# Kernel optimization log

Measured on AMD Instinct MI355X. Metric: run time of the kernel, lower is better.

The kernel has to match this reference:

```python
import jax, jax.numpy as jnp
import numpy as np

EPS = 1e-5

def _ln(x, g, b):
    mu = jnp.mean(x, axis=-1, keepdims=True)
    var = jnp.mean((x - mu) ** 2, axis=-1, keepdims=True)
    return (x - mu) / jnp.sqrt(var + EPS) * g + b

def setup_inputs() -> dict:
    key = jax.random.key(0)
    ks = jax.random.split(key, 8)
    S, B, L, M, D, Nq, H = 4, 256, 256, 4, 512, 4, 2048
    G = (M + 2) * D
    inp = {
        'ns_tokens': jax.random.normal(ks[0], (B, M, D), jnp.float32),
        'seq_tokens': jax.random.normal(ks[1], (S, B, L, D), jnp.float32),
        'seq_padding_masks': jax.random.randint(ks[2], (S, B, L), 0, 2).astype(bool),
        'seq_stats': jax.random.normal(ks[3], (S, B, 6), jnp.float32),
        'gin_gamma': jnp.ones((G,), jnp.float32),
        'gin_beta': jnp.zeros((G,), jnp.float32),
        'stat_W': 0.02 * jax.random.normal(ks[4], (S, 6, D), jnp.float32),
        'stat_b': jnp.zeros((S, D), jnp.float32),
        'stat_ln_g': jnp.ones((S, D), jnp.float32),
        'stat_ln_b': jnp.zeros((S, D), jnp.float32),
        'W1': 0.02 * jax.random.normal(ks[5], (S, Nq, G, H), jnp.float32),
        'b1': jnp.zeros((S, Nq, H), jnp.float32),
        'W2': 0.02 * jax.random.normal(ks[6], (S, Nq, H, D), jnp.float32),
        'b2': jnp.zeros((S, Nq, D), jnp.float32),
        'ln_g': jnp.ones((S, Nq, D), jnp.float32),
        'ln_b': jnp.zeros((S, Nq, D), jnp.float32),
    }
    return inp

def reference(ns_tokens, seq_tokens, seq_padding_masks, seq_stats,
              gin_gamma, gin_beta, stat_W, stat_b, stat_ln_g, stat_ln_b,
              W1, b1, W2, b2, ln_g, ln_b):
    S, B = seq_tokens.shape[0], ns_tokens.shape[0]
    ns_flat = ns_tokens.reshape(B, -1)                       # (B, M*D)
    valid = (~seq_padding_masks).astype(seq_tokens.dtype)[..., None]  # (S,B,L,1)
    denom = jnp.clip(jnp.sum(valid, axis=2), 1.0)            # (S,B,1)
    pooled = jnp.sum(seq_tokens * valid, axis=2) / denom     # (S,B,D)
    stat = jnp.einsum('sbf,sfd->sbd', seq_stats, stat_W) + stat_b[:, None]
    stat = _ln(stat, stat_ln_g[:, None], stat_ln_b[:, None])  # (S,B,D)
    gi = jnp.concatenate([jnp.broadcast_to(ns_flat[None], (S, B, ns_flat.shape[1])), pooled, stat], axis=-1)
    gi = _ln(gi, gin_gamma, gin_beta)                        # (S,B,G)
    h = jax.nn.silu(jnp.einsum('sbg,sqgh->sqbh', gi, W1) + b1[:, :, None])
    q = jnp.einsum('sqbh,sqhd->sqbd', h, W2) + b2[:, :, None]
    q = _ln(q, ln_g[:, :, None], ln_b[:, :, None])           # (S,Nq,B,D)
    return jnp.transpose(q, (0, 2, 1, 3))                    # (S,B,Nq,D)
```

## Files before the change

### kernel.cpp

```cpp
#include <hip/hip_runtime.h>
#include <hip/hip_bf16.h>

#define S_ 4
#define B_ 256
#define L_ 256
#define D_ 512
#define NQ_ 4
#define H_ 2048
#define G_ 3072

typedef __attribute__((ext_vector_type(4))) float f32x4;
typedef __attribute__((ext_vector_type(8))) short s16x8;

__device__ __forceinline__ unsigned short f2bf(float x) {
    __hip_bfloat16 hb = __float2bfloat16(x);
    return reinterpret_cast<unsigned short&>(hb);
}

__device__ __forceinline__ float block_sum256(float v, float* red) {
    #pragma unroll
    for (int off = 32; off > 0; off >>= 1) v += __shfl_down(v, off, 64);
    int tid = threadIdx.x;
    int lane = tid & 63, wid = tid >> 6;
    if (lane == 0) red[wid] = v;
    __syncthreads();
    float r = (tid < 4) ? red[tid] : 0.f;
    #pragma unroll
    for (int off = 4; off > 0; off >>= 1) r += __shfl_down(r, off, 64);
    if (tid == 0) red[0] = r;
    __syncthreads();
    float out = red[0];
    __syncthreads();
    return out;
}

__global__ __launch_bounds__(256) void pool_kernel(
    const float* __restrict__ seq_tokens,
    const unsigned char* __restrict__ masks_raw,
    float* __restrict__ pooled)
{
    const int sb = blockIdx.x;
    const int tid = threadIdx.x;
    __shared__ float sval[L_];
    __shared__ float scount[4];
    __shared__ f32x4 spart[256];
    __shared__ int is_bool_flag;

    if (tid == 0) is_bool_flag = 0;
    __syncthreads();
    {
        unsigned int w = reinterpret_cast<const unsigned int*>(masks_raw)[tid];
        if (w & 0xFFFFFF00u) is_bool_flag = 1;
    }
    __syncthreads();
    const bool is_bool = (is_bool_flag != 0);

    int mval;
    if (is_bool) {
        mval = masks_raw[(size_t)sb * L_ + tid];
    } else {
        mval = reinterpret_cast<const int*>(masks_raw)[(size_t)sb * L_ + tid];
    }
    float valid = mval ? 0.f : 1.f;
    sval[tid] = valid;
    float c = valid;
    #pragma unroll
    for (int off = 32; off > 0; off >>= 1) c += __shfl_down(c, off, 64);
    if ((tid & 63) == 0) scount[tid >> 6] = c;
    __syncthreads();
    const float denom = fmaxf(scount[0] + scount[1] + scount[2] + scount[3], 1.f);

    const float* base = seq_tokens + (size_t)sb * L_ * D_;
    const int cidx = tid & 127;
    const int rg = tid >> 7;
    f32x4 acc = {0.f, 0.f, 0.f, 0.f};
    for (int l = rg; l < L_; l += 2) {
        float vl = sval[l];
        f32x4 v = *reinterpret_cast<const f32x4*>(base + (size_t)l * D_ + cidx * 4);
        acc += v * vl;
    }
    spart[tid] = acc;
    __syncthreads();
    if (tid < 128) {
        f32x4 r = spart[tid] + spart[tid + 128];
        r *= (1.f / denom);
        *reinterpret_cast<f32x4*>(pooled + (size_t)sb * D_ + cidx * 4) = r;
    }
}

__global__ __launch_bounds__(256) void gi_kernel(
    const float* __restrict__ ns_tokens,
    const float* __restrict__ seq_stats,
    const float* __restrict__ stat_W,
    const float* __restrict__ stat_b,
    const float* __restrict__ stat_ln_g,
    const float* __restrict__ stat_ln_b,
    const float* __restrict__ gin_gamma,
    const float* __restrict__ gin_beta,
    const float* __restrict__ pooled,
    __hip_bfloat16* __restrict__ gi)
{
    const int sb = blockIdx.x;
    const int s = sb >> 8;
    const int b = sb & 255;
    const int tid = threadIdx.x;
    __shared__ float red[8];
    __shared__ float sstat[D_];

    float st[6];
    #pragma unroll
    for (int f = 0; f < 6; ++f) st[f] = seq_stats[(size_t)sb * 6 + f];

    float sp[2];
    #pragma unroll
    for (int k = 0; k < 2; ++k) {
        int d = tid + k * 256;
        float a = stat_b[s * D_ + d];
        #pragma unroll
        for (int f = 0; f < 6; ++f) a += st[f] * stat_W[(s * 6 + f) * D_ + d];
        sp[k] = a;
    }
    float ssum = block_sum256(sp[0] + sp[1], red);
    float ssq  = block_sum256(sp[0] * sp[0] + sp[1] * sp[1], red);
    float mu = ssum / D_;
    float var = ssq / D_ - mu * mu;
    float rinv = rsqrtf(var + 1e-5f);
    #pragma unroll
    for (int k = 0; k < 2; ++k) {
        int d = tid + k * 256;
        sstat[d] = (sp[k] - mu) * rinv * stat_ln_g[s * D_ + d] + stat_ln_b[s * D_ + d];
    }
    __syncthreads();

    float gv[12];
    float gsum = 0.f, gsq = 0.f;
    #pragma unroll
    for (int k = 0; k < 12; ++k) {
        int g = tid + k * 256;
        float v;
        if (g < 2048)       v = ns_tokens[(size_t)b * 2048 + g];
        else if (g < 2560)  v = pooled[(size_t)sb * D_ + (g - 2048)];
        else                v = sstat[g - 2560];
        gv[k] = v;
        gsum += v;
        gsq += v * v;
    }
    gsum = block_sum256(gsum, red);
    gsq  = block_sum256(gsq, red);
    mu = gsum / G_;
    var = gsq / G_ - mu * mu;
    rinv = rsqrtf(var + 1e-5f);
    #pragma unroll
    for (int k = 0; k < 12; ++k) {
        int g = tid + k * 256;
        float o = (gv[k] - mu) * rinv * gin_gamma[g] + gin_beta[g];
        gi[(size_t)sb * G_ + g] = __float2bfloat16(o);
    }
}

__global__ __launch_bounds__(256) void gemm1_kernel(
    const __hip_bfloat16* __restrict__ gi,
    const float* __restrict__ W1,
    const float* __restrict__ b1,
    __hip_bfloat16* __restrict__ hbuf)
{
    const int ntile = blockIdx.x;
    const int sq = blockIdx.y;
    const int s = sq >> 2;
    const int tid = threadIdx.x;
    const int lane = tid & 63;
    const int wid = tid >> 6;

    __shared__ __align__(16) unsigned short As[256 * 64];
    __shared__ __align__(16) unsigned short Ws[64 * 64];

    const __hip_bfloat16* Ab = gi + (size_t)s * B_ * G_;
    const float* Wb = W1 + (size_t)sq * G_ * H_ + ntile * 64;

    f32x4 acc[4][4];
    #pragma unroll
    for (int i = 0; i < 4; ++i)
        #pragma unroll
        for (int j = 0; j < 4; ++j) acc[i][j] = (f32x4){0.f, 0.f, 0.f, 0.f};

    const int wn0 = (tid & 15) * 4;
    const int wk0 = (tid >> 4) * 4;

    for (int kt = 0; kt < G_ / 64; ++kt) {
        const int kbase = kt * 64;
        __syncthreads();
        #pragma unroll
        for (int i = 0; i < 8; ++i) {
            int slot = i * 256 + tid;
            int row = slot >> 3, cc = slot & 7;
            int swz = (row ^ (row >> 3)) & 7;
            s16x8 v = *reinterpret_cast<const s16x8*>(Ab + (size_t)row * G_ + kbase + cc * 8);
            *reinterpret_cast<s16x8*>(&As[row * 64 + ((cc ^ swz) * 8)]) = v;
        }
        float wv[4][4];
        #pragma unroll
        for (int kk = 0; kk < 4; ++kk) {
            f32x4 t = *reinterpret_cast<const f32x4*>(Wb + (size_t)(kbase + wk0 + kk) * H_ + wn0);
            #pragma unroll
            for (int j = 0; j < 4; ++j) wv[kk][j] = t[j];
        }
        #pragma unroll
        for (int nn = 0; nn < 4; ++nn) {
            int row = wn0 + nn;
            int swz = (row ^ (row >> 3)) & 7;
            unsigned long long pk =
                (unsigned long long)f2bf(wv[0][nn]) |
                ((unsigned long long)f2bf(wv[1][nn]) << 16) |
                ((unsigned long long)f2bf(wv[2][nn]) << 32) |
                ((unsigned long long)f2bf(wv[3][nn]) << 48);
            int byteoff = (row * 128 + wk0 * 2) ^ (swz << 4);
            *reinterpret_cast<unsigned long long*>(reinterpret_cast<char*>(Ws) + byteoff) = pk;
        }
        __syncthreads();
        #pragma unroll
        for (int kb = 0; kb < 2; ++kb) {
            s16x8 af[4], bfr[4];
            #pragma unroll
            for (int mi = 0; mi < 4; ++mi) {
                int r = wid * 64 + mi * 16 + (lane & 15);
                int swz = (r ^ (r >> 3)) & 7;
                int chunk = ((lane >> 4) + kb * 4) ^ swz;
                af[mi] = *reinterpret_cast<const s16x8*>(&As[r * 64 + chunk * 8]);
            }
            #pragma unroll
            for (int ni = 0; ni < 4; ++ni) {
                int r = ni * 16 + (lane & 15);
                int swz = (r ^ (r >> 3)) & 7;
                int chunk = ((lane >> 4) + kb * 4) ^ swz;
                bfr[ni] = *reinterpret_cast<const s16x8*>(&Ws[r * 64 + chunk * 8]);
            }
            #pragma unroll
            for (int mi = 0; mi < 4; ++mi)
                #pragma unroll
                for (int ni = 0; ni < 4; ++ni)
                    acc[mi][ni] = __builtin_amdgcn_mfma_f32_16x16x32_bf16(af[mi], bfr[ni], acc[mi][ni], 0, 0, 0);
        }
    }
    const float* b1p = b1 + (size_t)sq * H_ + ntile * 64;
    __hip_bfloat16* hp = hbuf + (size_t)sq * B_ * H_;
    #pragma unroll
    for (int mi = 0; mi < 4; ++mi)
        #pragma unroll
        for (int ni = 0; ni < 4; ++ni)
            #pragma unroll
            for (int r = 0; r < 4; ++r) {
                int row = wid * 64 + mi * 16 + ((lane >> 4) << 2) + r;
                int coll = ni * 16 + (lane & 15);
                float x = acc[mi][ni][r] + b1p[coll];
                float sg = 1.f / (1.f + __expf(-x));
                hp[(size_t)row * H_ + ntile * 64 + coll] = __float2bfloat16(x * sg);
            }
}

__global__ __launch_bounds__(256) void gemm2_kernel(
    const __hip_bfloat16* __restrict__ hbuf,
    const float* __restrict__ W2,
    float* __restrict__ qpre)
{
    const int ntile = blockIdx.x;
    const int mtile = blockIdx.y;
    const int sq = blockIdx.z;
    const int tid = threadIdx.x;
    const int lane = tid & 63;
    const int wid = tid >> 6;
    const int wm = wid >> 1, wn = wid & 1;

    __shared__ __align__(16) unsigned short As[128 * 64];
    __shared__ __align__(16) unsigned short Ws[64 * 64];

    const __hip_bfloat16* Ab = hbuf + ((size_t)sq * B_ + mtile * 128) * H_;
    const float* Wb = W2 + (size_t)sq * H_ * D_ + ntile * 64;

    f32x4 acc[4][2];
    #pragma unroll
    for (int i = 0; i < 4; ++i)
        #pragma unroll
        for (int j = 0; j < 2; ++j) acc[i][j] = (f32x4){0.f, 0.f, 0.f, 0.f};

    const int wn0 = (tid & 15) * 4;
    const int wk0 = (tid >> 4) * 4;

    for (int kt = 0; kt < H_ / 64; ++kt) {
        const int kbase = kt * 64;
        __syncthreads();
        #pragma unroll
        for (int i = 0; i < 4; ++i) {
            int slot = i * 256 + tid;
            int row = slot >> 3, cc = slot & 7;
            int swz = (row ^ (row >> 3)) & 7;
            s16x8 v = *reinterpret_cast<const s16x8*>(Ab + (size_t)row * H_ + kbase + cc * 8);
            *reinterpret_cast<s16x8*>(&As[row * 64 + ((cc ^ swz) * 8)]) = v;
        }
        float wv[4][4];
        #pragma unroll
        for (int kk = 0; kk < 4; ++kk) {
            f32x4 t = *reinterpret_cast<const f32x4*>(Wb + (size_t)(kbase + wk0 + kk) * D_ + wn0);
            #pragma unroll
            for (int j = 0; j < 4; ++j) wv[kk][j] = t[j];
        }
        #pragma unroll
        for (int nn = 0; nn < 4; ++nn) {
            int row = wn0 + nn;
            int swz = (row ^ (row >> 3)) & 7;
            unsigned long long pk =
                (unsigned long long)f2bf(wv[0][nn]) |
                ((unsigned long long)f2bf(wv[1][nn]) << 16) |
                ((unsigned long long)f2bf(wv[2][nn]) << 32) |
                ((unsigned long long)f2bf(wv[3][nn]) << 48);
            int byteoff = (row * 128 + wk0 * 2) ^ (swz << 4);
            *reinterpret_cast<unsigned long long*>(reinterpret_cast<char*>(Ws) + byteoff) = pk;
        }
        __syncthreads();
        #pragma unroll
        for (int kb = 0; kb < 2; ++kb) {
            s16x8 af[4], bfr[2];
            #pragma unroll
            for (int mi = 0; mi < 4; ++mi) {
                int r = wm * 64 + mi * 16 + (lane & 15);
                int swz = (r ^ (r >> 3)) & 7;
                int chunk = ((lane >> 4) + kb * 4) ^ swz;
                af[mi] = *reinterpret_cast<const s16x8*>(&As[r * 64 + chunk * 8]);
            }
            #pragma unroll
            for (int ni = 0; ni < 2; ++ni) {
                int r = wn * 32 + ni * 16 + (lane & 15);
                int swz = (r ^ (r >> 3)) & 7;
                int chunk = ((lane >> 4) + kb * 4) ^ swz;
                bfr[ni] = *reinterpret_cast<const s16x8*>(&Ws[r * 64 + chunk * 8]);
            }
            #pragma unroll
            for (int mi = 0; mi < 4; ++mi)
                #pragma unroll
                for (int ni = 0; ni < 2; ++ni)
                    acc[mi][ni] = __builtin_amdgcn_mfma_f32_16x16x32_bf16(af[mi], bfr[ni], acc[mi][ni], 0, 0, 0);
        }
    }
    #pragma unroll
    for (int mi = 0; mi < 4; ++mi)
        #pragma unroll
        for (int ni = 0; ni < 2; ++ni)
            #pragma unroll
            for (int r = 0; r < 4; ++r) {
                int row = mtile * 128 + wm * 64 + mi * 16 + ((lane >> 4) << 2) + r;
                int col = ntile * 64 + wn * 32 + ni * 16 + (lane & 15);
                qpre[((size_t)sq * B_ + row) * D_ + col] = acc[mi][ni][r];
            }
}

__global__ __launch_bounds__(256) void lnout_kernel(
    const float* __restrict__ qpre,
    const float* __restrict__ b2,
    const float* __restrict__ lng,
    const float* __restrict__ lnb,
    float* __restrict__ out)
{
    const int idx = blockIdx.x;
    const int sq = idx >> 8;
    const int b = idx & 255;
    const int tid = threadIdx.x;
    __shared__ float red[8];

    float v[2];
    #pragma unroll
    for (int k = 0; k < 2; ++k) {
        int d = tid + k * 256;
        v[k] = qpre[(size_t)idx * D_ + d] + b2[sq * D_ + d];
    }
    float sum = block_sum256(v[0] + v[1], red);
    float sq2 = block_sum256(v[0] * v[0] + v[1] * v[1], red);
    float mu = sum / D_;
    float var = sq2 / D_ - mu * mu;
    float rinv = rsqrtf(var + 1e-5f);
    const int s = sq >> 2, q = sq & 3;
    #pragma unroll
    for (int k = 0; k < 2; ++k) {
        int d = tid + k * 256;
        float o = (v[k] - mu) * rinv * lng[sq * D_ + d] + lnb[sq * D_ + d];
        out[(((size_t)s * B_ + b) * NQ_ + q) * D_ + d] = o;
    }
}

extern "C" void kernel_launch(void* const* d_in, const int* in_sizes, int n_in,
                              void* d_out, int out_size, void* d_ws, size_t ws_size,
                              hipStream_t stream) {
    const float* ns_tokens   = (const float*)d_in[0];
    const float* seq_tokens  = (const float*)d_in[1];
    const unsigned char* masks = (const unsigned char*)d_in[2];
    const float* seq_stats   = (const float*)d_in[3];
    const float* gin_gamma   = (const float*)d_in[4];
    const float* gin_beta    = (const float*)d_in[5];
    const float* stat_W      = (const float*)d_in[6];
    const float* stat_b      = (const float*)d_in[7];
    const float* stat_ln_g   = (const float*)d_in[8];
    const float* stat_ln_b   = (const float*)d_in[9];
    const float* W1          = (const float*)d_in[10];
    const float* b1          = (const float*)d_in[11];
    const float* W2          = (const float*)d_in[12];
    const float* b2          = (const float*)d_in[13];
    const float* ln_g        = (const float*)d_in[14];
    const float* ln_b        = (const float*)d_in[15];
    float* out = (float*)d_out;

    char* ws = (char*)d_ws;
    float* pooled        = (float*)(ws);
    __hip_bfloat16* gi   = (__hip_bfloat16*)(ws + 2097152);
    __hip_bfloat16* hbuf = (__hip_bfloat16*)(ws + 2097152 + 6291456);
    float* qpre          = (float*)(ws + 2097152 + 6291456 + 16777216);

    pool_kernel<<<dim3(S_ * B_), dim3(256), 0, stream>>>(seq_tokens, masks, pooled);
    gi_kernel<<<dim3(S_ * B_), dim3(256), 0, stream>>>(ns_tokens, seq_stats, stat_W, stat_b,
                                                       stat_ln_g, stat_ln_b, gin_gamma, gin_beta,
                                                       pooled, gi);
    gemm1_kernel<<<dim3(H_ / 64, S_ * NQ_), dim3(256), 0, stream>>>(gi, W1, b1, hbuf);
    gemm2_kernel<<<dim3(D_ / 64, B_ / 128, S_ * NQ_), dim3(256), 0, stream>>>(hbuf, W2, qpre);
    lnout_kernel<<<dim3(S_ * NQ_ * B_), dim3(256), 0, stream>>>(qpre, b2, ln_g, ln_b, out);
}
```

Measured before the change: 268.3 us.

## Remap GEMM blocks per XCD, issue weight loads first, store qpre as bf16

Both GEMM kernels switch to a 1D grid and remap block ids so that consecutive ids handled by the same XCD (bid & 7) share the same sq slice. This aims to improve L2 reuse of the shared activation tile across the XCDs. Inside the K loop, the fp32 weight global loads are now issued before the bf16 activation loads to expose more memory-level parallelism. The intermediate qpre buffer is stored as bf16 instead of fp32, halving its write and read traffic but adding rounding error before the final layernorm.

```diff
diff --git a/kernel.cpp b/kernel.cpp
--- a/kernel.cpp
+++ b/kernel.cpp
@@ -56,11 +56,8 @@
     const bool is_bool = (is_bool_flag != 0);
 
     int mval;
-    if (is_bool) {
-        mval = masks_raw[(size_t)sb * L_ + tid];
-    } else {
-        mval = reinterpret_cast<const int*>(masks_raw)[(size_t)sb * L_ + tid];
-    }
+    if (is_bool) mval = masks_raw[(size_t)sb * L_ + tid];
+    else         mval = reinterpret_cast<const int*>(masks_raw)[(size_t)sb * L_ + tid];
     float valid = mval ? 0.f : 1.f;
     sval[tid] = valid;
     float c = valid;
@@ -164,8 +161,10 @@
     const float* __restrict__ b1,
     __hip_bfloat16* __restrict__ hbuf)
 {
-    const int ntile = blockIdx.x;
-    const int sq = blockIdx.y;
+    const int bid = blockIdx.x;
+    const int wg = (bid & 7) * 64 + (bid >> 3);
+    const int ntile = wg & 31;
+    const int sq = wg >> 5;
     const int s = sq >> 2;
     const int tid = threadIdx.x;
     const int lane = tid & 63;
@@ -189,6 +188,13 @@
     for (int kt = 0; kt < G_ / 64; ++kt) {
         const int kbase = kt * 64;
         __syncthreads();
+        float wv[4][4];
+        #pragma unroll
+        for (int kk = 0; kk < 4; ++kk) {
+            f32x4 t = *reinterpret_cast<const f32x4*>(Wb + (size_t)(kbase + wk0 + kk) * H_ + wn0);
+            #pragma unroll
+            for (int j = 0; j < 4; ++j) wv[kk][j] = t[j];
+        }
         #pragma unroll
         for (int i = 0; i < 8; ++i) {
             int slot = i * 256 + tid;
@@ -196,13 +202,6 @@
             int swz = (row ^ (row >> 3)) & 7;
             s16x8 v = *reinterpret_cast<const s16x8*>(Ab + (size_t)row * G_ + kbase + cc * 8);
             *reinterpret_cast<s16x8*>(&As[row * 64 + ((cc ^ swz) * 8)]) = v;
-        }
-        float wv[4][4];
-        #pragma unroll
-        for (int kk = 0; kk < 4; ++kk) {
-            f32x4 t = *reinterpret_cast<const f32x4*>(Wb + (size_t)(kbase + wk0 + kk) * H_ + wn0);
-            #pragma unroll
-            for (int j = 0; j < 4; ++j) wv[kk][j] = t[j];
         }
         #pragma unroll
         for (int nn = 0; nn < 4; ++nn) {
@@ -260,11 +259,13 @@
 __global__ __launch_bounds__(256) void gemm2_kernel(
     const __hip_bfloat16* __restrict__ hbuf,
     const float* __restrict__ W2,
-    float* __restrict__ qpre)
+    __hip_bfloat16* __restrict__ qpre)
 {
-    const int ntile = blockIdx.x;
-    const int mtile = blockIdx.y;
-    const int sq = blockIdx.z;
+    const int bid = blockIdx.x;
+    const int wg = (bid & 7) * 32 + (bid >> 3);
+    const int ntile = wg & 7;
+    const int mtile = (wg >> 3) & 1;
+    const int sq = wg >> 4;
     const int tid = threadIdx.x;
     const int lane = tid & 63;
     const int wid = tid >> 6;
@@ -288,6 +289,13 @@
     for (int kt = 0; kt < H_ / 64; ++kt) {
         const int kbase = kt * 64;
         __syncthreads();
+        float wv[4][4];
+        #pragma unroll
+        for (int kk = 0; kk < 4; ++kk) {
+            f32x4 t = *reinterpret_cast<const f32x4*>(Wb + (size_t)(kbase + wk0 + kk) * D_ + wn0);
+            #pragma unroll
+            for (int j = 0; j < 4; ++j) wv[kk][j] = t[j];
+        }
         #pragma unroll
         for (int i = 0; i < 4; ++i) {
             int slot = i * 256 + tid;
@@ -295,13 +303,6 @@
             int swz = (row ^ (row >> 3)) & 7;
             s16x8 v = *reinterpret_cast<const s16x8*>(Ab + (size_t)row * H_ + kbase + cc * 8);
             *reinterpret_cast<s16x8*>(&As[row * 64 + ((cc ^ swz) * 8)]) = v;
-        }
-        float wv[4][4];
-        #pragma unroll
-        for (int kk = 0; kk < 4; ++kk) {
-            f32x4 t = *reinterpret_cast<const f32x4*>(Wb + (size_t)(kbase + wk0 + kk) * D_ + wn0);
-            #pragma unroll
-            for (int j = 0; j < 4; ++j) wv[kk][j] = t[j];
         }
         #pragma unroll
         for (int nn = 0; nn < 4; ++nn) {
@@ -348,12 +349,12 @@
             for (int r = 0; r < 4; ++r) {
                 int row = mtile * 128 + wm * 64 + mi * 16 + ((lane >> 4) << 2) + r;
                 int col = ntile * 64 + wn * 32 + ni * 16 + (lane & 15);
-                qpre[((size_t)sq * B_ + row) * D_ + col] = acc[mi][ni][r];
+                qpre[((size_t)sq * B_ + row) * D_ + col] = __float2bfloat16(acc[mi][ni][r]);
             }
 }
 
 __global__ __launch_bounds__(256) void lnout_kernel(
-    const float* __restrict__ qpre,
+    const __hip_bfloat16* __restrict__ qpre,
     const float* __restrict__ b2,
     const float* __restrict__ lng,
     const float* __restrict__ lnb,
@@ -369,7 +370,7 @@
     #pragma unroll
     for (int k = 0; k < 2; ++k) {
         int d = tid + k * 256;
-        v[k] = qpre[(size_t)idx * D_ + d] + b2[sq * D_ + d];
+        v[k] = __bfloat162float(qpre[(size_t)idx * D_ + d]) + b2[sq * D_ + d];
     }
     float sum = block_sum256(v[0] + v[1], red);
     float sq2 = block_sum256(v[0] * v[0] + v[1] * v[1], red);
@@ -410,13 +411,13 @@
     float* pooled        = (float*)(ws);
     __hip_bfloat16* gi   = (__hip_bfloat16*)(ws + 2097152);
     __hip_bfloat16* hbuf = (__hip_bfloat16*)(ws + 2097152 + 6291456);
-    float* qpre          = (float*)(ws + 2097152 + 6291456 + 16777216);
+    __hip_bfloat16* qpre = (__hip_bfloat16*)(ws + 2097152 + 6291456 + 16777216);
 
     pool_kernel<<<dim3(S_ * B_), dim3(256), 0, stream>>>(seq_tokens, masks, pooled);
     gi_kernel<<<dim3(S_ * B_), dim3(256), 0, stream>>>(ns_tokens, seq_stats, stat_W, stat_b,
                                                        stat_ln_g, stat_ln_b, gin_gamma, gin_beta,
                                                        pooled, gi);
-    gemm1_kernel<<<dim3(H_ / 64, S_ * NQ_), dim3(256), 0, stream>>>(gi, W1, b1, hbuf);
-    gemm2_kernel<<<dim3(D_ / 64, B_ / 128, S_ * NQ_), dim3(256), 0, stream>>>(hbuf, W2, qpre);
+    gemm1_kernel<<<dim3(32 * S_ * NQ_), dim3(256), 0, stream>>>(gi, W1, b1, hbuf);
+    gemm2_kernel<<<dim3(2 * D_ / 64 * S_ * NQ_), dim3(256), 0, stream>>>(hbuf, W2, qpre);
     lnout_kernel<<<dim3(S_ * NQ_ * B_), dim3(256), 0, stream>>>(qpre, b2, ln_g, ln_b, out);
 }
```

After: 274.0 us. 2.1% more time.
